# Kernel optimization log

Measured on AMD Instinct MI355X. Metric: run time of the kernel, lower is better.

Reference implementation:

```python
import jax, jax.numpy as jnp
import numpy as np
from jax import lax

EPS = 1e-5
TRUNK_C, REG_C, GPOOL_C = 256, 192, 64
B, H, W = 256, 19, 19


def setup_inputs() -> dict:
    key = jax.random.key(0)
    ks = jax.random.split(key, 18)
    def bn_params(k, c):
        k1, k2, k3, k4 = jax.random.split(k, 4)
        return (jax.random.normal(k1, (c,)) * 0.1 + 1.0,   # gamma
                jax.random.normal(k2, (c,)) * 0.1,          # beta
                jax.random.normal(k3, (c,)) * 0.1,          # running mean
                jax.random.uniform(k4, (c,)) * 0.5 + 0.5)   # running var
    bn1_g, bn1_b, bn1_m, bn1_v = bn_params(ks[0], TRUNK_C)
    bn1b_g, bn1b_b, bn1b_m, bn1b_v = bn_params(ks[1], GPOOL_C)
    bn2_g, bn2_b, bn2_m, bn2_v = bn_params(ks[2], REG_C)
    x = jax.random.normal(ks[3], (B, TRUNK_C, H, W), dtype=jnp.float32)
    w1a = jax.random.normal(ks[4], (REG_C, TRUNK_C, 3, 3), dtype=jnp.float32) * (1.0 / np.sqrt(TRUNK_C * 9))
    w1b = jax.random.normal(ks[5], (GPOOL_C, TRUNK_C, 3, 3), dtype=jnp.float32) * (1.0 / np.sqrt(TRUNK_C * 9))
    w_lin = jax.random.normal(ks[6], (REG_C, 3 * GPOOL_C), dtype=jnp.float32) * (1.0 / np.sqrt(3 * GPOOL_C))
    w2 = jax.random.normal(ks[7], (TRUNK_C, REG_C, 3, 3), dtype=jnp.float32) * (1.0 / np.sqrt(REG_C * 9))
    return {
        'x': x, 'bn1_g': bn1_g, 'bn1_b': bn1_b, 'bn1_m': bn1_m, 'bn1_v': bn1_v,
        'w1a': w1a, 'w1b': w1b,
        'bn1b_g': bn1b_g, 'bn1b_b': bn1b_b, 'bn1b_m': bn1b_m, 'bn1b_v': bn1b_v,
        'w_lin': w_lin,
        'bn2_g': bn2_g, 'bn2_b': bn2_b, 'bn2_m': bn2_m, 'bn2_v': bn2_v,
        'w2': w2,
    }


def _bn(x, g, b, m, v):
    # inference batchnorm over channel dim of NCHW
    inv = g / jnp.sqrt(v + EPS)
    return (x - m[:, None, None]) * inv[:, None, None] + b[:, None, None]


def _mish(x):
    return x * jnp.tanh(jax.nn.softplus(x))


def _conv(x, w):
    return lax.conv_general_dilated(x, w, (1, 1), 'SAME',
                                    dimension_numbers=('NCHW', 'OIHW', 'NCHW'))


def _kata_gpool(x):
    # x: [B, C, H, W] -> [B, 3C]: mean, mean*(sqrt(N)-14)/10, max
    b, c, h, w = x.shape
    n = float(h * w)
    sqrt_n = n ** 0.5
    mean = jnp.sum(x, axis=(2, 3)) / n
    max_val = jnp.max(x, axis=(2, 3))
    scaled_mean = mean * ((sqrt_n - 14.0) / 10.0)
    return jnp.concatenate([mean, scaled_mean, max_val], axis=1)


def reference(x, bn1_g, bn1_b, bn1_m, bn1_v, w1a, w1b,
              bn1b_g, bn1b_b, bn1b_m, bn1b_v, w_lin,
              bn2_g, bn2_b, bn2_m, bn2_v, w2):
    out = _mish(_bn(x, bn1_g, bn1_b, bn1_m, bn1_v))
    reg = _conv(out, w1a)                       # [B, REG_C, H, W]
    gp = _conv(out, w1b)                        # [B, GPOOL_C, H, W]
    gp = _mish(_bn(gp, bn1b_g, bn1b_b, bn1b_m, bn1b_v))
    gp_pooled = _kata_gpool(gp)                 # [B, 3*GPOOL_C]
    gp_out = gp_pooled @ w_lin.T                # [B, REG_C]
    reg = reg + gp_out[:, :, None, None]
    out2 = _mish(_bn(reg, bn2_g, bn2_b, bn2_m, bn2_v))
    out2 = _conv(out2, w2)
    return out2 + x
```

## Files before the change

### kernel.cpp

```cpp
#include <hip/hip_runtime.h>
#include <hip/hip_bf16.h>
#include <math.h>


#define BATCH   256
#define TRUNK_C 256
#define REG_C   192
#define GPOOL_C 64
#define HH      19
#define WW      19
#define HW      361
#define PP      441
#define EPS     1e-5f

typedef __hip_bfloat16 bf16;
typedef __attribute__((ext_vector_type(8))) short short8;
typedef __attribute__((ext_vector_type(4))) float floatx4;

__device__ __forceinline__ float b2f(bf16 v) { return __bfloat162float(v); }
__device__ __forceinline__ bf16  f2b(float v) { return __float2bfloat16(v); }

__device__ __forceinline__ float mish_f(float v) {
    if (v > 20.0f) return v;
    float u = __expf(v);
    float n = u * (u + 2.0f);
    return v * __fdividef(n, n + 2.0f);
}

__device__ __forceinline__ void gload_lds16(const void* gsrc, void* lds) {
    __builtin_amdgcn_global_load_lds(
        (const __attribute__((address_space(1))) void*)gsrc,
        (__attribute__((address_space(3))) void*)lds, 16, 0, 0);
}

__global__ void prep_kernel(
    const float* g1, const float* b1, const float* m1, const float* v1,
    const float* g1b, const float* b1b, const float* m1b, const float* v1b,
    const float* g2, const float* b2, const float* m2, const float* v2,
    const float* __restrict__ w1a, const float* __restrict__ w1b,
    const float* __restrict__ w2,
    bf16* __restrict__ w1c_p, bf16* __restrict__ w2_p,
    bf16* __restrict__ act_pad, bf16* __restrict__ reg_pad,
    float* bnbuf)
{
    const int T1  = 16 * 72 * 64 * 8;
    const int T2  = 16 * 54 * 64 * 8;
    const int TW  = T1 + T2;
    const int TBa = BATCH * 80 * 32;
    const int TBr = BATCH * 80 * 24;
    int i = blockIdx.x * blockDim.x + threadIdx.x;
    if (i < TW) {
        if (i < T1) {
            int j = i & 7, lane = (i >> 3) & 63;
            int kc = (i >> 9) % 72, cog = (i >> 9) / 72;
            int co = cog * 16 + (lane & 15);
            int k = kc * 32 + ((lane >> 4) << 3) + j;
            int r = k >> 8, ci = k & 255;
            float v = (co < 192) ? w1a[co * 2304 + ci * 9 + r]
                                 : w1b[(co - 192) * 2304 + ci * 9 + r];
            w1c_p[i] = f2b(v);
        } else {
            int i2 = i - T1;
            int j = i2 & 7, lane = (i2 >> 3) & 63;
            int kc = (i2 >> 9) % 54, cog = (i2 >> 9) / 54;
            int co = cog * 16 + (lane & 15);
            int k = kc * 32 + ((lane >> 4) << 3) + j;
            int r = k / 192, ci = k % 192;
            w2_p[i2] = f2b(w2[co * 1728 + ci * 9 + r]);
        }
    } else if (i < TW + TBa + TBr) {
        int j = i - TW;
        bool isact = j < TBa;
        if (!isact) j -= TBa;
        int nb = isact ? 32 : 24;
        int b = j / (80 * nb);
        int rem = j - b * (80 * nb);
        int e = rem / nb, g = rem - (rem / nb) * nb;
        int pp;
        if (e < 21) pp = e;
        else if (e < 42) pp = 420 + (e - 21);
        else if (e < 61) pp = (e - 41) * 21;
        else pp = (e - 60) * 21 + 20;
        short8 z = {0, 0, 0, 0, 0, 0, 0, 0};
        if (isact) *(short8*)(act_pad + ((size_t)b * PP + pp) * TRUNK_C + g * 8) = z;
        else       *(short8*)(reg_pad + ((size_t)b * PP + pp) * REG_C + g * 8) = z;
    } else {
        int t = i - (TW + TBa + TBr);
        if (t < 256) {
            float s = g1[t] / sqrtf(v1[t] + EPS);
            bnbuf[t] = s;
            bnbuf[256 + t] = b1[t] - m1[t] * s;
        } else if (t < 320) {
            int c = t - 256;
            float s = g1b[c] / sqrtf(v1b[c] + EPS);
            bnbuf[512 + c] = s;
            bnbuf[576 + c] = b1b[c] - m1b[c] * s;
        } else if (t < 512) {
            int c = t - 320;
            float s = g2[c] / sqrtf(v2[c] + EPS);
            bnbuf[640 + c] = s;
            bnbuf[832 + c] = b2[c] - m2[c] * s;
        }
    }
}

__global__ __launch_bounds__(256)
void bn1_mish_t_kernel(const float* __restrict__ x, const float* __restrict__ bnbuf,
                       bf16* __restrict__ act_pad) {
    __shared__ float lds[256][32];
    int pc = blockIdx.x;
    int b  = blockIdx.y;
    int t  = threadIdx.x;
    int p0 = pc * 32;
    int px = t & 31;
#pragma unroll
    for (int it = 0; it < 32; ++it) {
        int ci = it * 8 + (t >> 5);
        int p  = p0 + px;
        float v = 0.0f;
        if (p < HW) v = x[((size_t)b * TRUNK_C + ci) * HW + p];
        v = v * bnbuf[ci] + bnbuf[256 + ci];
        lds[ci][px ^ (ci >> 3)] = mish_f(v);
    }
    __syncthreads();
#pragma unroll
    for (int it = 0; it < 4; ++it) {
        int pl = it * 8 + (t >> 5);
        int p  = p0 + pl;
        if (p >= HW) continue;
        int ch = t & 31;
        short8 vv;
#pragma unroll
        for (int j = 0; j < 8; ++j) {
            bf16 h = f2b(lds[ch * 8 + j][pl ^ ch]);
            short s;
            __builtin_memcpy(&s, &h, 2);
            vv[j] = s;
        }
        int pp = (p / WW + 1) * 21 + (p % WW + 1);
        *(short8*)(act_pad + ((size_t)b * PP + pp) * TRUNK_C + ch * 8) = vv;
    }
}

__global__ __launch_bounds__(256, 3)
void conv1_kernel(const bf16* __restrict__ act,
                  const bf16* __restrict__ wfrag,
                  bf16* __restrict__ reg_out,
                  bf16* __restrict__ gp_out,
                  const float* __restrict__ ep_scale, const float* __restrict__ ep_bias) {
    const int CIN = 256, NKC = 72;
    __shared__ __align__(16) bf16 atile[4][128 * 32];
    const int b   = blockIdx.x;
    const int mt  = blockIdx.y;
    const int nh  = blockIdx.z;
    const int t   = threadIdx.x;
    const int w   = t >> 6, lane = t & 63;
    const int mi  = w >> 1, ni = w & 1;
    const int l15 = lane & 15, quad = lane >> 4;

    int row0 = t >> 2;
    int sq   = t & 3;
    int ss   = sq ^ ((row0 >> 1) & 3);
    int sp0  = mt * 128 + row0;      if (sp0 > 360) sp0 = 360;
    int sp1  = mt * 128 + row0 + 64; if (sp1 > 360) sp1 = 360;
    const bf16* sb0 = act + ((size_t)b * PP + (sp0 / WW) * 21 + (sp0 % WW)) * CIN + (ss << 3);
    const bf16* sb1 = act + ((size_t)b * PP + (sp1 / WW) * 21 + (sp1 % WW)) * CIN + (ss << 3);

    const bf16* wb[4];
#pragma unroll
    for (int ns = 0; ns < 4; ++ns)
        wb[ns] = wfrag + ((size_t)(nh * 8 + ni * 4 + ns) * NKC * 64 + lane) * 8;

    int aoff[4];
#pragma unroll
    for (int ms = 0; ms < 4; ++ms) {
        int row = mi * 64 + ms * 16 + l15;
        aoff[ms] = row * 32 + ((quad ^ ((row >> 1) & 3)) << 3);
    }

    auto stage = [&](int buf, int kc) {
        int r = kc >> 3, c = kc & 7;
        int off = ((r / 3) * 21 + (r % 3)) * CIN + (c << 5);
        bf16* dst = &atile[buf][w << 9];
        gload_lds16(sb0 + off, dst);
        gload_lds16(sb1 + off, dst + 2048);
    };

    floatx4 acc[4][4];
#pragma unroll
    for (int i = 0; i < 4; ++i)
#pragma unroll
        for (int j = 0; j < 4; ++j) acc[i][j] = (floatx4){0.f, 0.f, 0.f, 0.f};

    short8 afr[4], bfrA[4], bfrB[4];
    stage(0, 0);
    stage(1, 1);
    asm volatile("" ::: "memory");
#pragma unroll
    for (int ns = 0; ns < 4; ++ns) bfrA[ns] = *(const short8*)(wb[ns]);
    asm volatile("" ::: "memory");
    stage(2, 2);

    for (int kc = 0; kc < NKC; kc += 2) {
        if (kc == 0) asm volatile("s_waitcnt vmcnt(8)" ::: "memory");
        else         asm volatile("s_waitcnt vmcnt(12)" ::: "memory");
        __builtin_amdgcn_sched_barrier(0);
        __builtin_amdgcn_s_barrier();
        __builtin_amdgcn_sched_barrier(0);
#pragma unroll
        for (int ns = 0; ns < 4; ++ns)
            bfrB[ns] = *(const short8*)(wb[ns] + (size_t)(kc + 1) * 512);
        asm volatile("" ::: "memory");
        {
            int s = kc + 3; if (s > NKC - 1) s = NKC - 1;
            stage((kc + 3) & 3, s);
        }
        {
            const bf16* at = atile[kc & 3];
#pragma unroll
            for (int ms = 0; ms < 4; ++ms)
                afr[ms] = *(const short8*)(at + aoff[ms]);
        }
#pragma unroll
        for (int ms = 0; ms < 4; ++ms)
#pragma unroll
            for (int ns = 0; ns < 4; ++ns)
                acc[ms][ns] = __builtin_amdgcn_mfma_f32_16x16x32_bf16(
                    afr[ms], bfrA[ns], acc[ms][ns], 0, 0, 0);

        asm volatile("s_waitcnt vmcnt(12)" ::: "memory");
        __builtin_amdgcn_sched_barrier(0);
        __builtin_amdgcn_s_barrier();
        __builtin_amdgcn_sched_barrier(0);
        {
            int nb = kc + 2; if (nb > NKC - 1) nb = NKC - 1;
#pragma unroll
            for (int ns = 0; ns < 4; ++ns)
                bfrA[ns] = *(const short8*)(wb[ns] + (size_t)nb * 512);
        }
        asm volatile("" ::: "memory");
        {
            int s = kc + 4; if (s > NKC - 1) s = NKC - 1;
            stage((kc + 4) & 3, s);
        }
        {
            const bf16* at = atile[(kc + 1) & 3];
#pragma unroll
            for (int ms = 0; ms < 4; ++ms)
                afr[ms] = *(const short8*)(at + aoff[ms]);
        }
#pragma unroll
        for (int ms = 0; ms < 4; ++ms)
#pragma unroll
            for (int ns = 0; ns < 4; ++ns)
                acc[ms][ns] = __builtin_amdgcn_mfma_f32_16x16x32_bf16(
                    afr[ms], bfrB[ns], acc[ms][ns], 0, 0, 0);
    }

    float scl[4], bia[4];
#pragma unroll
    for (int ns = 0; ns < 4; ++ns) {
        int co = (nh * 8 + ni * 4 + ns) * 16 + l15;
        if (co >= 192) { scl[ns] = ep_scale[co - 192]; bia[ns] = ep_bias[co - 192]; }
    }
#pragma unroll
    for (int ms = 0; ms < 4; ++ms) {
#pragma unroll
        for (int rg = 0; rg < 4; ++rg) {
            int p = mt * 128 + mi * 64 + ms * 16 + quad * 4 + rg;
            if (p > 360) continue;
            size_t ppad = (size_t)b * PP + (p / WW + 1) * 21 + (p % WW + 1);
#pragma unroll
            for (int ns = 0; ns < 4; ++ns) {
                int co = (nh * 8 + ni * 4 + ns) * 16 + l15;
                float v = acc[ms][ns][rg];
                if (co < 192) {
                    reg_out[ppad * REG_C + co] = f2b(v);
                } else {
                    v = mish_f(v * scl[ns] + bia[ns]);
                    gp_out[((size_t)b * HW + p) * GPOOL_C + (co - 192)] = f2b(v);
                }
            }
        }
    }
}

__global__ __launch_bounds__(256, 3)
void conv2_kernel(const bf16* __restrict__ act,
                  const bf16* __restrict__ wfrag,
                  const float* __restrict__ resid,
                  float* __restrict__ out) {
    const int CIN = 192, NKC = 54;
    __shared__ __align__(16) bf16 atile[4][128 * 32];
    const int b   = blockIdx.x;
    const int mt  = blockIdx.y;
    const int nh  = blockIdx.z;
    const int t   = threadIdx.x;
    const int w   = t >> 6, lane = t & 63;
    const int pw  = w >> 1, cw = w & 1;
    const int l15 = lane & 15, quad = lane >> 4;

    int row0 = t >> 2;
    int sq   = t & 3;
    int ss   = sq ^ ((row0 >> 1) & 3);
    int sp0  = mt * 128 + row0;      if (sp0 > 360) sp0 = 360;
    int sp1  = mt * 128 + row0 + 64; if (sp1 > 360) sp1 = 360;
    const bf16* sb0 = act + ((size_t)b * PP + (sp0 / WW) * 21 + (sp0 % WW)) * CIN + (ss << 3);
    const bf16* sb1 = act + ((size_t)b * PP + (sp1 / WW) * 21 + (sp1 % WW)) * CIN + (ss << 3);

    const bf16* wb[4];
#pragma unroll
    for (int ms = 0; ms < 4; ++ms)
        wb[ms] = wfrag + ((size_t)(nh * 8 + cw * 4 + ms) * NKC * 64 + lane) * 8;

    int aoff[4];
#pragma unroll
    for (int ns = 0; ns < 4; ++ns) {
        int row = pw * 64 + ns * 16 + l15;
        aoff[ns] = row * 32 + ((quad ^ ((row >> 1) & 3)) << 3);
    }

    auto stage = [&](int buf, int kc) {
        int r = kc / 6, c = kc % 6;
        int off = ((r / 3) * 21 + (r % 3)) * CIN + (c << 5);
        bf16* dst = &atile[buf][w << 9];
        gload_lds16(sb0 + off, dst);
        gload_lds16(sb1 + off, dst + 2048);
    };

    floatx4 acc[4][4];
#pragma unroll
    for (int i = 0; i < 4; ++i)
#pragma unroll
        for (int j = 0; j < 4; ++j) acc[i][j] = (floatx4){0.f, 0.f, 0.f, 0.f};

    short8 bfa[4], wfrA[4], wfrB[4];
    stage(0, 0);
    stage(1, 1);
    asm volatile("" ::: "memory");
#pragma unroll
    for (int ms = 0; ms < 4; ++ms) wfrA[ms] = *(const short8*)(wb[ms]);
    asm volatile("" ::: "memory");
    stage(2, 2);

    for (int kc = 0; kc < NKC; kc += 2) {
        if (kc == 0) asm volatile("s_waitcnt vmcnt(8)" ::: "memory");
        else         asm volatile("s_waitcnt vmcnt(12)" ::: "memory");
        __builtin_amdgcn_sched_barrier(0);
        __builtin_amdgcn_s_barrier();
        __builtin_amdgcn_sched_barrier(0);
#pragma unroll
        for (int ms = 0; ms < 4; ++ms)
            wfrB[ms] = *(const short8*)(wb[ms] + (size_t)(kc + 1) * 512);
        asm volatile("" ::: "memory");
        {
            int s = kc + 3; if (s > NKC - 1) s = NKC - 1;
            stage((kc + 3) & 3, s);
        }
        {
            const bf16* at = atile[kc & 3];
#pragma unroll
            for (int ns = 0; ns < 4; ++ns)
                bfa[ns] = *(const short8*)(at + aoff[ns]);
        }
#pragma unroll
        for (int ms = 0; ms < 4; ++ms)
#pragma unroll
            for (int ns = 0; ns < 4; ++ns)
                acc[ms][ns] = __builtin_amdgcn_mfma_f32_16x16x32_bf16(
                    wfrA[ms], bfa[ns], acc[ms][ns], 0, 0, 0);

        asm volatile("s_waitcnt vmcnt(12)" ::: "memory");
        __builtin_amdgcn_sched_barrier(0);
        __builtin_amdgcn_s_barrier();
        __builtin_amdgcn_sched_barrier(0);
        {
            int nb = kc + 2; if (nb > NKC - 1) nb = NKC - 1;
#pragma unroll
            for (int ms = 0; ms < 4; ++ms)
                wfrA[ms] = *(const short8*)(wb[ms] + (size_t)nb * 512);
        }
        asm volatile("" ::: "memory");
        {
            int s = kc + 4; if (s > NKC - 1) s = NKC - 1;
            stage((kc + 4) & 3, s);
        }
        {
            const bf16* at = atile[(kc + 1) & 3];
#pragma unroll
            for (int ns = 0; ns < 4; ++ns)
                bfa[ns] = *(const short8*)(at + aoff[ns]);
        }
#pragma unroll
        for (int ms = 0; ms < 4; ++ms)
#pragma unroll
            for (int ns = 0; ns < 4; ++ns)
                acc[ms][ns] = __builtin_amdgcn_mfma_f32_16x16x32_bf16(
                    wfrB[ms], bfa[ns], acc[ms][ns], 0, 0, 0);
    }

#pragma unroll
    for (int ns = 0; ns < 4; ++ns) {
        int p = mt * 128 + pw * 64 + ns * 16 + l15;
        if (p > 360) continue;
#pragma unroll
        for (int ms = 0; ms < 4; ++ms) {
#pragma unroll
            for (int rg = 0; rg < 4; ++rg) {
                int co = (nh * 8 + cw * 4 + ms) * 16 + quad * 4 + rg;
                size_t idx = ((size_t)b * TRUNK_C + co) * HW + p;
                out[idx] = acc[ms][ns][rg] + resid[idx];
            }
        }
    }
}

__global__ void gpool_lin_kernel(const bf16* __restrict__ gp, const float* __restrict__ w_lin,
                                 float* __restrict__ gpout) {
    __shared__ float ls[4][64], lm[4][64];
    __shared__ float pooled_s[192];
    int b = blockIdx.x;
    int t = threadIdx.x;
    int c = t & 63, sub = t >> 6;
    float s = 0.0f, mx = -1e30f;
    for (int p = sub; p < HW; p += 4) {
        float v = b2f(gp[((size_t)b * HW + p) * GPOOL_C + c]);
        s += v;
        mx = fmaxf(mx, v);
    }
    ls[sub][c] = s; lm[sub][c] = mx;
    __syncthreads();
    if (t < 64) {
        float ss = ls[0][t] + ls[1][t] + ls[2][t] + ls[3][t];
        float mm = fmaxf(fmaxf(lm[0][t], lm[1][t]), fmaxf(lm[2][t], lm[3][t]));
        float mean = ss * (1.0f / 361.0f);
        pooled_s[t] = mean;
        pooled_s[64 + t] = mean * 0.5f;
        pooled_s[128 + t] = mm;
    }
    __syncthreads();
    if (t < 192) {
        const float4* wr4 = (const float4*)(w_lin + t * 192);
        float acc = 0.0f;
#pragma unroll 8
        for (int j = 0; j < 48; ++j) {
            float4 wv = wr4[j];
            acc = fmaf(pooled_s[j * 4 + 0], wv.x, acc);
            acc = fmaf(pooled_s[j * 4 + 1], wv.y, acc);
            acc = fmaf(pooled_s[j * 4 + 2], wv.z, acc);
            acc = fmaf(pooled_s[j * 4 + 3], wv.w, acc);
        }
        gpout[b * 192 + t] = acc;
    }
}

__global__ __launch_bounds__(256)
void add_bn2_mish_kernel(bf16* __restrict__ reg_pad, const float* __restrict__ gpout,
                         const float* __restrict__ bnbuf) {
    const int total = BATCH * HW * 24;
    int i = blockIdx.x * blockDim.x + threadIdx.x;
    if (i >= total) return;
    int g  = i % 24;
    int bp = i / 24;
    int p  = bp % HW;
    int b  = bp / HW;
    int pp = (p / WW + 1) * 21 + (p % WW + 1);
    size_t idx = ((size_t)b * PP + pp) * REG_C + g * 8;
    short8 v = *(const short8*)(reg_pad + idx);
    const float* gpo = gpout + b * 192 + g * 8;
    const float* sc  = bnbuf + 640 + g * 8;
    const float* bi  = bnbuf + 832 + g * 8;
    short8 o;
#pragma unroll
    for (int j = 0; j < 8; ++j) {
        short sj = v[j];
        bf16 h;
        __builtin_memcpy(&h, &sj, 2);
        float f = b2f(h) + gpo[j];
        f = f * sc[j] + bi[j];
        h = f2b(mish_f(f));
        __builtin_memcpy(&sj, &h, 2);
        o[j] = sj;
    }
    *(short8*)(reg_pad + idx) = o;
}

extern "C" void kernel_launch(void* const* d_in, const int* in_sizes, int n_in,
                              void* d_out, int out_size, void* d_ws, size_t ws_size,
                              hipStream_t stream) {
    const float* x     = (const float*)d_in[0];
    const float* bn1_g = (const float*)d_in[1];
    const float* bn1_b = (const float*)d_in[2];
    const float* bn1_m = (const float*)d_in[3];
    const float* bn1_v = (const float*)d_in[4];
    const float* w1a   = (const float*)d_in[5];
    const float* w1b   = (const float*)d_in[6];
    const float* bn1b_g = (const float*)d_in[7];
    const float* bn1b_b = (const float*)d_in[8];
    const float* bn1b_m = (const float*)d_in[9];
    const float* bn1b_v = (const float*)d_in[10];
    const float* w_lin  = (const float*)d_in[11];
    const float* bn2_g  = (const float*)d_in[12];
    const float* bn2_b  = (const float*)d_in[13];
    const float* bn2_m  = (const float*)d_in[14];
    const float* bn2_v  = (const float*)d_in[15];
    const float* w2     = (const float*)d_in[16];
    float* out = (float*)d_out;

    char* ws = (char*)d_ws;
    size_t off = 0;
    auto alloc = [&](size_t bytes) {
        void* p = ws + off;
        off += (bytes + 255) & ~(size_t)255;
        return p;
    };
    bf16*  act_pad = (bf16*)alloc((size_t)BATCH * PP * TRUNK_C * sizeof(bf16));
    bf16*  reg_pad = (bf16*)alloc((size_t)BATCH * PP * REG_C * sizeof(bf16));
    bf16*  gp      = (bf16*)alloc((size_t)BATCH * HW * GPOOL_C * sizeof(bf16));
    bf16*  w1c_p   = (bf16*)alloc((size_t)16 * 72 * 64 * 8 * sizeof(bf16));
    bf16*  w2_p    = (bf16*)alloc((size_t)16 * 54 * 64 * 8 * sizeof(bf16));
    float* gpout   = (float*)alloc((size_t)BATCH * 192 * sizeof(float));
    float* bnbuf   = (float*)alloc(1024 * sizeof(float));
    (void)ws_size;

    {
        const int total = (16 * 72 * 64 * 8) + (16 * 54 * 64 * 8)
                        + BATCH * 80 * 32 + BATCH * 80 * 24 + 512;
        hipLaunchKernelGGL(prep_kernel, dim3((total + 255) / 256), dim3(256), 0, stream,
                           bn1_g, bn1_b, bn1_m, bn1_v,
                           bn1b_g, bn1b_b, bn1b_m, bn1b_v,
                           bn2_g, bn2_b, bn2_m, bn2_v,
                           w1a, w1b, w2, w1c_p, w2_p, act_pad, reg_pad, bnbuf);
    }

    hipLaunchKernelGGL(bn1_mish_t_kernel, dim3(12, BATCH), dim3(256), 0, stream,
                       x, bnbuf, act_pad);

    hipLaunchKernelGGL(conv1_kernel, dim3(BATCH, 3, 2), dim3(256), 0, stream,
                       act_pad, w1c_p, reg_pad, gp, bnbuf + 512, bnbuf + 576);

    hipLaunchKernelGGL(gpool_lin_kernel, dim3(BATCH), dim3(256), 0, stream,
                       gp, w_lin, gpout);

    {
        int total = BATCH * HW * 24;
        hipLaunchKernelGGL(add_bn2_mish_kernel, dim3((total + 255) / 256), dim3(256), 0, stream,
                           reg_pad, gpout, bnbuf);
    }

    hipLaunchKernelGGL(conv2_kernel, dim3(BATCH, 3, 2), dim3(256), 0, stream,
                       reg_pad, w2_p, x, out);
}
```

Baseline: 669.2 us.

## Restructure conv pipelines, remap workgroups, fuse gpool with bn2-mish

Both conv kernels now wait at one barrier per two k-steps and issue two stage loads at once. They raise wave priority around the MFMA blocks and decode a flat 1D grid so that work groups sharing a batch run close together. The gpool/linear kernel and the add+bn2+mish elementwise kernel are merged into one per-batch kernel that folds the pooled bias into the BN affine, which removes the gpout buffer and a launch. Risks are a reduced prefetch depth from dropping stage(2,2) before the loop, lower parallelism in the fused elementwise pass (256 blocks), and possible LDS buffer hazards with a single barrier per iteration.

```diff
diff --git a/kernel.cpp b/kernel.cpp
--- a/kernel.cpp
+++ b/kernel.cpp
@@ -142,6 +142,14 @@
     }
 }
 
+__device__ __forceinline__ void decode_wg(int wg, int& b, int& mt, int& nh) {
+    int g = wg >> 4, r = wg & 15;
+    nh = r >> 3;
+    int pr = (g << 3) | (r & 7);
+    b = pr / 3;
+    mt = pr - b * 3;
+}
+
 __global__ __launch_bounds__(256, 3)
 void conv1_kernel(const bf16* __restrict__ act,
                   const bf16* __restrict__ wfrag,
@@ -150,9 +158,8 @@
                   const float* __restrict__ ep_scale, const float* __restrict__ ep_bias) {
     const int CIN = 256, NKC = 72;
     __shared__ __align__(16) bf16 atile[4][128 * 32];
-    const int b   = blockIdx.x;
-    const int mt  = blockIdx.y;
-    const int nh  = blockIdx.z;
+    int b, mt, nh;
+    decode_wg(blockIdx.x, b, mt, nh);
     const int t   = threadIdx.x;
     const int w   = t >> 6, lane = t & 63;
     const int mi  = w >> 1, ni = w & 1;
@@ -198,40 +205,38 @@
     asm volatile("" ::: "memory");
 #pragma unroll
     for (int ns = 0; ns < 4; ++ns) bfrA[ns] = *(const short8*)(wb[ns]);
-    asm volatile("" ::: "memory");
-    stage(2, 2);
 
     for (int kc = 0; kc < NKC; kc += 2) {
-        if (kc == 0) asm volatile("s_waitcnt vmcnt(8)" ::: "memory");
-        else         asm volatile("s_waitcnt vmcnt(12)" ::: "memory");
+        if (kc == 0) asm volatile("s_waitcnt vmcnt(4)" ::: "memory");
+        else         asm volatile("s_waitcnt vmcnt(8)" ::: "memory");
         __builtin_amdgcn_sched_barrier(0);
         __builtin_amdgcn_s_barrier();
         __builtin_amdgcn_sched_barrier(0);
+        {
+            int s0 = kc + 2; if (s0 > NKC - 1) s0 = NKC - 1;
+            int s1 = kc + 3; if (s1 > NKC - 1) s1 = NKC - 1;
+            stage((kc + 2) & 3, s0);
+            stage((kc + 3) & 3, s1);
+        }
+        asm volatile("" ::: "memory");
 #pragma unroll
         for (int ns = 0; ns < 4; ++ns)
             bfrB[ns] = *(const short8*)(wb[ns] + (size_t)(kc + 1) * 512);
         asm volatile("" ::: "memory");
         {
-            int s = kc + 3; if (s > NKC - 1) s = NKC - 1;
-            stage((kc + 3) & 3, s);
-        }
-        {
             const bf16* at = atile[kc & 3];
 #pragma unroll
             for (int ms = 0; ms < 4; ++ms)
                 afr[ms] = *(const short8*)(at + aoff[ms]);
         }
+        __builtin_amdgcn_s_setprio(1);
 #pragma unroll
         for (int ms = 0; ms < 4; ++ms)
 #pragma unroll
             for (int ns = 0; ns < 4; ++ns)
                 acc[ms][ns] = __builtin_amdgcn_mfma_f32_16x16x32_bf16(
                     afr[ms], bfrA[ns], acc[ms][ns], 0, 0, 0);
-
-        asm volatile("s_waitcnt vmcnt(12)" ::: "memory");
-        __builtin_amdgcn_sched_barrier(0);
-        __builtin_amdgcn_s_barrier();
-        __builtin_amdgcn_sched_barrier(0);
+        __builtin_amdgcn_s_setprio(0);
         {
             int nb = kc + 2; if (nb > NKC - 1) nb = NKC - 1;
 #pragma unroll
@@ -239,22 +244,20 @@
                 bfrA[ns] = *(const short8*)(wb[ns] + (size_t)nb * 512);
         }
         asm volatile("" ::: "memory");
-        {
-            int s = kc + 4; if (s > NKC - 1) s = NKC - 1;
-            stage((kc + 4) & 3, s);
-        }
         {
             const bf16* at = atile[(kc + 1) & 3];
 #pragma unroll
             for (int ms = 0; ms < 4; ++ms)
                 afr[ms] = *(const short8*)(at + aoff[ms]);
         }
+        __builtin_amdgcn_s_setprio(1);
 #pragma unroll
         for (int ms = 0; ms < 4; ++ms)
 #pragma unroll
             for (int ns = 0; ns < 4; ++ns)
                 acc[ms][ns] = __builtin_amdgcn_mfma_f32_16x16x32_bf16(
                     afr[ms], bfrB[ns], acc[ms][ns], 0, 0, 0);
+        __builtin_amdgcn_s_setprio(0);
     }
 
     float scl[4], bia[4];
@@ -292,9 +295,8 @@
                   float* __restrict__ out) {
     const int CIN = 192, NKC = 54;
     __shared__ __align__(16) bf16 atile[4][128 * 32];
-    const int b   = blockIdx.x;
-    const int mt  = blockIdx.y;
-    const int nh  = blockIdx.z;
+    int b, mt, nh;
+    decode_wg(blockIdx.x, b, mt, nh);
     const int t   = threadIdx.x;
     const int w   = t >> 6, lane = t & 63;
     const int pw  = w >> 1, cw = w & 1;
@@ -340,40 +342,38 @@
     asm volatile("" ::: "memory");
 #pragma unroll
     for (int ms = 0; ms < 4; ++ms) wfrA[ms] = *(const short8*)(wb[ms]);
-    asm volatile("" ::: "memory");
-    stage(2, 2);
 
     for (int kc = 0; kc < NKC; kc += 2) {
-        if (kc == 0) asm volatile("s_waitcnt vmcnt(8)" ::: "memory");
-        else         asm volatile("s_waitcnt vmcnt(12)" ::: "memory");
+        if (kc == 0) asm volatile("s_waitcnt vmcnt(4)" ::: "memory");
+        else         asm volatile("s_waitcnt vmcnt(8)" ::: "memory");
         __builtin_amdgcn_sched_barrier(0);
         __builtin_amdgcn_s_barrier();
         __builtin_amdgcn_sched_barrier(0);
+        {
+            int s0 = kc + 2; if (s0 > NKC - 1) s0 = NKC - 1;
+            int s1 = kc + 3; if (s1 > NKC - 1) s1 = NKC - 1;
+            stage((kc + 2) & 3, s0);
+            stage((kc + 3) & 3, s1);
+        }
+        asm volatile("" ::: "memory");
 #pragma unroll
         for (int ms = 0; ms < 4; ++ms)
             wfrB[ms] = *(const short8*)(wb[ms] + (size_t)(kc + 1) * 512);
         asm volatile("" ::: "memory");
         {
-            int s = kc + 3; if (s > NKC - 1) s = NKC - 1;
-            stage((kc + 3) & 3, s);
-        }
-        {
             const bf16* at = atile[kc & 3];
 #pragma unroll
             for (int ns = 0; ns < 4; ++ns)
                 bfa[ns] = *(const short8*)(at + aoff[ns]);
         }
+        __builtin_amdgcn_s_setprio(1);
 #pragma unroll
         for (int ms = 0; ms < 4; ++ms)
 #pragma unroll
             for (int ns = 0; ns < 4; ++ns)
                 acc[ms][ns] = __builtin_amdgcn_mfma_f32_16x16x32_bf16(
                     wfrA[ms], bfa[ns], acc[ms][ns], 0, 0, 0);
-
-        asm volatile("s_waitcnt vmcnt(12)" ::: "memory");
-        __builtin_amdgcn_sched_barrier(0);
-        __builtin_amdgcn_s_barrier();
-        __builtin_amdgcn_sched_barrier(0);
+        __builtin_amdgcn_s_setprio(0);
         {
             int nb = kc + 2; if (nb > NKC - 1) nb = NKC - 1;
 #pragma unroll
@@ -382,21 +382,19 @@
         }
         asm volatile("" ::: "memory");
         {
-            int s = kc + 4; if (s > NKC - 1) s = NKC - 1;
-            stage((kc + 4) & 3, s);
-        }
-        {
             const bf16* at = atile[(kc + 1) & 3];
 #pragma unroll
             for (int ns = 0; ns < 4; ++ns)
                 bfa[ns] = *(const short8*)(at + aoff[ns]);
         }
+        __builtin_amdgcn_s_setprio(1);
 #pragma unroll
         for (int ms = 0; ms < 4; ++ms)
 #pragma unroll
             for (int ns = 0; ns < 4; ++ns)
                 acc[ms][ns] = __builtin_amdgcn_mfma_f32_16x16x32_bf16(
                     wfrB[ms], bfa[ns], acc[ms][ns], 0, 0, 0);
+        __builtin_amdgcn_s_setprio(0);
     }
 
 #pragma unroll
@@ -415,10 +413,13 @@
     }
 }
 
-__global__ void gpool_lin_kernel(const bf16* __restrict__ gp, const float* __restrict__ w_lin,
-                                 float* __restrict__ gpout) {
+__global__ __launch_bounds__(256)
+void gpool_bn2_kernel(const bf16* __restrict__ gp, const float* __restrict__ w_lin,
+                      const float* __restrict__ bnbuf, bf16* __restrict__ reg_pad) {
     __shared__ float ls[4][64], lm[4][64];
     __shared__ float pooled_s[192];
+    __shared__ float gob_s[192];
+    __shared__ float s2_s[192];
     int b = blockIdx.x;
     int t = threadIdx.x;
     int c = t & 63, sub = t >> 6;
@@ -450,39 +451,30 @@
             acc = fmaf(pooled_s[j * 4 + 2], wv.z, acc);
             acc = fmaf(pooled_s[j * 4 + 3], wv.w, acc);
         }
-        gpout[b * 192 + t] = acc;
-    }
-}
-
-__global__ __launch_bounds__(256)
-void add_bn2_mish_kernel(bf16* __restrict__ reg_pad, const float* __restrict__ gpout,
-                         const float* __restrict__ bnbuf) {
-    const int total = BATCH * HW * 24;
-    int i = blockIdx.x * blockDim.x + threadIdx.x;
-    if (i >= total) return;
-    int g  = i % 24;
-    int bp = i / 24;
-    int p  = bp % HW;
-    int b  = bp / HW;
-    int pp = (p / WW + 1) * 21 + (p % WW + 1);
-    size_t idx = ((size_t)b * PP + pp) * REG_C + g * 8;
-    short8 v = *(const short8*)(reg_pad + idx);
-    const float* gpo = gpout + b * 192 + g * 8;
-    const float* sc  = bnbuf + 640 + g * 8;
-    const float* bi  = bnbuf + 832 + g * 8;
-    short8 o;
-#pragma unroll
-    for (int j = 0; j < 8; ++j) {
-        short sj = v[j];
-        bf16 h;
-        __builtin_memcpy(&h, &sj, 2);
-        float f = b2f(h) + gpo[j];
-        f = f * sc[j] + bi[j];
-        h = f2b(mish_f(f));
-        __builtin_memcpy(&sj, &h, 2);
-        o[j] = sj;
-    }
-    *(short8*)(reg_pad + idx) = o;
+        float s2 = bnbuf[640 + t];
+        s2_s[t]  = s2;
+        gob_s[t] = acc * s2 + bnbuf[832 + t];
+    }
+    __syncthreads();
+    for (int i = t; i < HW * 24; i += 256) {
+        int p = i / 24, g = i - (i / 24) * 24;
+        int pp = (p / WW + 1) * 21 + (p % WW + 1);
+        size_t idx = ((size_t)b * PP + pp) * REG_C + g * 8;
+        short8 v = *(const short8*)(reg_pad + idx);
+        short8 o;
+#pragma unroll
+        for (int j = 0; j < 8; ++j) {
+            int cc = g * 8 + j;
+            short sj = v[j];
+            bf16 h;
+            __builtin_memcpy(&h, &sj, 2);
+            float f = b2f(h) * s2_s[cc] + gob_s[cc];
+            h = f2b(mish_f(f));
+            __builtin_memcpy(&sj, &h, 2);
+            o[j] = sj;
+        }
+        *(short8*)(reg_pad + idx) = o;
+    }
 }
 
 extern "C" void kernel_launch(void* const* d_in, const int* in_sizes, int n_in,
@@ -519,7 +511,6 @@
     bf16*  gp      = (bf16*)alloc((size_t)BATCH * HW * GPOOL_C * sizeof(bf16));
     bf16*  w1c_p   = (bf16*)alloc((size_t)16 * 72 * 64 * 8 * sizeof(bf16));
     bf16*  w2_p    = (bf16*)alloc((size_t)16 * 54 * 64 * 8 * sizeof(bf16));
-    float* gpout   = (float*)alloc((size_t)BATCH * 192 * sizeof(float));
     float* bnbuf   = (float*)alloc(1024 * sizeof(float));
     (void)ws_size;
 
@@ -536,18 +527,12 @@
     hipLaunchKernelGGL(bn1_mish_t_kernel, dim3(12, BATCH), dim3(256), 0, stream,
                        x, bnbuf, act_pad);
 
-    hipLaunchKernelGGL(conv1_kernel, dim3(BATCH, 3, 2), dim3(256), 0, stream,
+    hipLaunchKernelGGL(conv1_kernel, dim3(1536), dim3(256), 0, stream,
                        act_pad, w1c_p, reg_pad, gp, bnbuf + 512, bnbuf + 576);
 
-    hipLaunchKernelGGL(gpool_lin_kernel, dim3(BATCH), dim3(256), 0, stream,
-                       gp, w_lin, gpout);
-
-    {
-        int total = BATCH * HW * 24;
-        hipLaunchKernelGGL(add_bn2_mish_kernel, dim3((total + 255) / 256), dim3(256), 0, stream,
-                           reg_pad, gpout, bnbuf);
-    }
-
-    hipLaunchKernelGGL(conv2_kernel, dim3(BATCH, 3, 2), dim3(256), 0, stream,
+    hipLaunchKernelGGL(gpool_bn2_kernel, dim3(BATCH), dim3(256), 0, stream,
+                       gp, w_lin, bnbuf, reg_pad);
+
+    hipLaunchKernelGGL(conv2_kernel, dim3(1536), dim3(256), 0, stream,
                        reg_pad, w2_p, x, out);
 }
```

Result: faster. 563.8 us (-15.7%).
